# Optimization experiments

Measured on AMD Instinct MI355X. Metric: run time of the kernel, lower is better.

Reference implementation:

```python
import jax, jax.numpy as jnp
import numpy as np

B, D_IN, D_H = 8192, 2048, 2048


def _glorot(key, shape, fan_in):
    bound = 1.0 / np.sqrt(fan_in)
    return jax.random.uniform(key, shape, jnp.float32, -bound, bound)


def setup_inputs() -> dict:
    key = jax.random.key(0)
    ks = jax.random.split(key, 16)
    inp = {
        'x': jax.random.normal(ks[0], (B, D_IN), jnp.float32),
        'h': jax.random.normal(ks[1], (B, D_H), jnp.float32),
        'c': jax.random.normal(ks[2], (B, D_H), jnp.float32),
    }
    # Linear weights stored torch-style: W [out, in], y = x @ W.T + b
    names = ['Wix', 'Wmx', 'Wox']
    for i, n in enumerate(names):
        inp[n] = _glorot(ks[3 + i], (D_H, D_IN), D_IN)
        inp['b' + n[1:]] = _glorot(ks[6 + i], (D_H,), D_IN)
    names_h = ['Wih', 'Wmh', 'Woh']
    for i, n in enumerate(names_h):
        inp[n] = _glorot(ks[9 + i], (D_H, D_H), D_H)
        inp['b' + n[1:]] = _glorot(ks[12 + i], (D_H,), D_H)
    return inp


def reference(x, h, c, Wix, bix, Wmx, bmx, Wox, box, Wih, bih, Wmh, bmh, Woh, boh):
    # Fuse the 3 distinct x-GEMMs and 3 h-GEMMs into two concatenated GEMMs.
    Wx = jnp.concatenate([Wix, Wmx, Wox], axis=0)   # [3H, D_IN]
    Wh = jnp.concatenate([Wih, Wmh, Woh], axis=0)   # [3H, D_H]
    bx = jnp.concatenate([bix, bmx, box])
    bh = jnp.concatenate([bih, bmh, boh])
    g = x @ Wx.T + bx + h @ Wh.T + bh               # [B, 3H]
    gi, gm, go = jnp.split(g, 3, axis=-1)
    input_state = jax.nn.sigmoid(gi)
    # Faithful to source: memory gate pre-activation used for BOTH
    # the sigmoid "forget" gate and the tanh candidate (forgot_gate_* unused).
    forgot_state = jax.nn.sigmoid(gm)
    memory_state = jnp.tanh(gm)
    output_state = jax.nn.sigmoid(go)
    c_new = forgot_state * c + input_state * memory_state
    h_new = output_state * jnp.tanh(c_new)
    return (h_new, c_new)
```

## Files before the change

kernel.cpp:

```cpp
#include <hip/hip_runtime.h>

#define DEV __device__ __forceinline__

typedef __bf16 bf16x8 __attribute__((ext_vector_type(8)));
typedef float f32x4 __attribute__((ext_vector_type(4)));
typedef unsigned short ushort8 __attribute__((ext_vector_type(8)));

constexpr int BATCH = 8192;
constexpr int HD    = 2048;
constexpr size_t NX   = (size_t)BATCH * HD;
constexpr size_t NW   = (size_t)HD * HD;
constexpr size_t NTOT = 2 * NX + 6 * NW;

DEV unsigned short f2bf(float f) {
    unsigned int v = __builtin_bit_cast(unsigned int, f);
    unsigned int r = (v + 0x7FFFu + ((v >> 16) & 1u)) >> 16;
    return (unsigned short)r;
}
DEV float sigm(float v)  { return 1.0f / (1.0f + __expf(-v)); }
DEV float tanh_(float v) {
    float z = fminf(fmaxf(v, -15.0f), 15.0f);
    float e = __expf(2.0f * z);
    return (e - 1.0f) / (e + 1.0f);
}

DEV void gl16(const unsigned short* g, unsigned short* lds_uniform_base) {
    __builtin_amdgcn_global_load_lds(
        (const __attribute__((address_space(1))) unsigned int*)g,
        (__attribute__((address_space(3))) unsigned int*)lds_uniform_base,
        16, 0, 0);
}

struct CvtArgs { const float* src[8]; };

__global__ __launch_bounds__(256) void cvt_all(CvtArgs a, unsigned short* __restrict__ dst) {
    const size_t starts[9] = {0, NX, 2*NX, 2*NX+NW, 2*NX+2*NW, 2*NX+3*NW,
                              2*NX+4*NW, 2*NX+5*NW, NTOT};
    const size_t base = (size_t)blockIdx.x * 2048;
    int s = 0;
    while (base >= starts[s + 1]) ++s;
    const float* src = a.src[s] + (base - starts[s]) + threadIdx.x * 8;
    f32x4 u0 = *reinterpret_cast<const f32x4*>(src);
    f32x4 u1 = *reinterpret_cast<const f32x4*>(src + 4);
    ushort8 v;
#pragma unroll
    for (int j = 0; j < 4; ++j) { v[j] = f2bf(u0[j]); v[4 + j] = f2bf(u1[j]); }
    *reinterpret_cast<ushort8*>(dst + base + threadIdx.x * 8) = v;
}

__global__ __launch_bounds__(256, 2) void lstm_fast(
    const unsigned short* __restrict__ xb, const unsigned short* __restrict__ hb,
    const unsigned short* __restrict__ W0x, const unsigned short* __restrict__ W1x,
    const unsigned short* __restrict__ W2x, const unsigned short* __restrict__ W0h,
    const unsigned short* __restrict__ W1h, const unsigned short* __restrict__ W2h,
    const float* __restrict__ c,
    const float* __restrict__ bix, const float* __restrict__ bih,
    const float* __restrict__ bmx, const float* __restrict__ bmh,
    const float* __restrict__ box_, const float* __restrict__ boh,
    float* __restrict__ hout, float* __restrict__ cout)
{
    __shared__ unsigned short As [128 * 32];
    __shared__ unsigned short B0s[128 * 32];
    __shared__ unsigned short B1s[128 * 32];
    __shared__ unsigned short B2s[128 * 32];

    const int tid  = threadIdx.x;
    const int lane = tid & 63;
    const int wave = tid >> 6;

    const int n0 = blockIdx.x * 128;
    const int m0 = blockIdx.y * 128;

    const int arow = lane >> 2;
    const int acol = (lane & 3) * 8;

    const int mOff = (wave >> 1) * 64;
    const int nOff = (wave & 1) * 64;
    const int q    = lane >> 4;
    const int ml   = lane & 15;

    f32x4 a0[4][4] = {};
    f32x4 a1[4][4] = {};
    f32x4 a2[4][4] = {};

    const int r0 = wave * 32, r1 = wave * 32 + 16;

    for (int kt = 0; kt < 128; ++kt) {
        const int k0 = kt * 32;
        const unsigned short *Asrc, *W0, *W1, *W2;
        int kk;
        if (k0 < HD) { Asrc = xb; W0 = W0x; W1 = W1x; W2 = W2x; kk = k0; }
        else         { Asrc = hb; W0 = W0h; W1 = W1h; W2 = W2h; kk = k0 - HD; }

        gl16(Asrc + (size_t)(m0 + r0 + arow) * HD + kk + acol, &As [r0 * 32]);
        gl16(Asrc + (size_t)(m0 + r1 + arow) * HD + kk + acol, &As [r1 * 32]);
        gl16(W0   + (size_t)(n0 + r0 + arow) * HD + kk + acol, &B0s[r0 * 32]);
        gl16(W0   + (size_t)(n0 + r1 + arow) * HD + kk + acol, &B0s[r1 * 32]);
        gl16(W1   + (size_t)(n0 + r0 + arow) * HD + kk + acol, &B1s[r0 * 32]);
        gl16(W1   + (size_t)(n0 + r1 + arow) * HD + kk + acol, &B1s[r1 * 32]);
        gl16(W2   + (size_t)(n0 + r0 + arow) * HD + kk + acol, &B2s[r0 * 32]);
        gl16(W2   + (size_t)(n0 + r1 + arow) * HD + kk + acol, &B2s[r1 * 32]);
        __syncthreads();

        bf16x8 af[4];
#pragma unroll
        for (int t = 0; t < 4; ++t)
            af[t] = *reinterpret_cast<const bf16x8*>(&As[(mOff + t * 16 + ml) * 32 + q * 8]);

        {
            bf16x8 bfr[4];
#pragma unroll
            for (int tn = 0; tn < 4; ++tn)
                bfr[tn] = *reinterpret_cast<const bf16x8*>(&B0s[(nOff + tn * 16 + ml) * 32 + q * 8]);
#pragma unroll
            for (int tm = 0; tm < 4; ++tm)
#pragma unroll
                for (int tn = 0; tn < 4; ++tn)
                    a0[tm][tn] = __builtin_amdgcn_mfma_f32_16x16x32_bf16(af[tm], bfr[tn], a0[tm][tn], 0, 0, 0);
        }
        {
            bf16x8 bfr[4];
#pragma unroll
            for (int tn = 0; tn < 4; ++tn)
                bfr[tn] = *reinterpret_cast<const bf16x8*>(&B1s[(nOff + tn * 16 + ml) * 32 + q * 8]);
#pragma unroll
            for (int tm = 0; tm < 4; ++tm)
#pragma unroll
                for (int tn = 0; tn < 4; ++tn)
                    a1[tm][tn] = __builtin_amdgcn_mfma_f32_16x16x32_bf16(af[tm], bfr[tn], a1[tm][tn], 0, 0, 0);
        }
        {
            bf16x8 bfr[4];
#pragma unroll
            for (int tn = 0; tn < 4; ++tn)
                bfr[tn] = *reinterpret_cast<const bf16x8*>(&B2s[(nOff + tn * 16 + ml) * 32 + q * 8]);
#pragma unroll
            for (int tm = 0; tm < 4; ++tm)
#pragma unroll
                for (int tn = 0; tn < 4; ++tn)
                    a2[tm][tn] = __builtin_amdgcn_mfma_f32_16x16x32_bf16(af[tm], bfr[tn], a2[tm][tn], 0, 0, 0);
        }
        __syncthreads();
    }

#pragma unroll
    for (int tn = 0; tn < 4; ++tn) {
        const int col = n0 + nOff + tn * 16 + ml;
        const float Bi = bix[col] + bih[col];
        const float Bm = bmx[col] + bmh[col];
        const float Bo = box_[col] + boh[col];
#pragma unroll
        for (int tm = 0; tm < 4; ++tm) {
            const int rb = m0 + mOff + tm * 16 + q * 4;
#pragma unroll
            for (int r = 0; r < 4; ++r) {
                const size_t b = rb + r;
                const float cold = c[b * HD + col];
                const float gi = a0[tm][tn][r] + Bi;
                const float gm = a1[tm][tn][r] + Bm;
                const float go = a2[tm][tn][r] + Bo;
                const float i_s = sigm(gi);
                const float f_s = sigm(gm);
                const float m_s = tanh_(gm);
                const float o_s = sigm(go);
                const float cn  = f_s * cold + i_s * m_s;
                const float hn  = o_s * tanh_(cn);
                hout[b * HD + col] = hn;
                cout[b * HD + col] = cn;
            }
        }
    }
}

DEV void stage64f(unsigned short* lds, const float* src, size_t row_base, int kk, int tid) {
    const int r  = tid >> 2;
    const int cc = (tid & 3) * 8;
    const float* s = src + (row_base + r) * (size_t)HD + kk + cc;
    f32x4 u0 = *(const f32x4*)s;
    f32x4 u1 = *(const f32x4*)(s + 4);
    ushort8 v;
#pragma unroll
    for (int j = 0; j < 4; ++j) { v[j] = f2bf(u0[j]); v[4 + j] = f2bf(u1[j]); }
    *reinterpret_cast<ushort8*>(&lds[r * 32 + cc]) = v;
}

__global__ __launch_bounds__(256, 2) void lstm_slow(
    const float* __restrict__ x,   const float* __restrict__ h,
    const float* __restrict__ c,
    const float* __restrict__ Wix, const float* __restrict__ bix,
    const float* __restrict__ Wmx, const float* __restrict__ bmx,
    const float* __restrict__ Wox, const float* __restrict__ box_,
    const float* __restrict__ Wih, const float* __restrict__ bih,
    const float* __restrict__ Wmh, const float* __restrict__ bmh,
    const float* __restrict__ Woh, const float* __restrict__ boh,
    float* __restrict__ hout, float* __restrict__ cout)
{
    __shared__ unsigned short As[64 * 32];
    __shared__ unsigned short B0s[128 * 32];
    __shared__ unsigned short B1s[128 * 32];
    __shared__ unsigned short B2s[128 * 32];

    const int tid  = threadIdx.x;
    const int lane = tid & 63;
    const int wave = tid >> 6;
    const int n0 = blockIdx.x * 128;
    const int m0 = blockIdx.y * 64;
    const int mOff = (wave >> 1) * 32;
    const int nOff = (wave & 1) * 64;
    const int q    = lane >> 4;
    const int ml   = lane & 15;

    f32x4 a0[2][4] = {}; f32x4 a1[2][4] = {}; f32x4 a2[2][4] = {};

    auto kstep = [&](const float* Asrc, const float* W0, const float* W1,
                     const float* W2, int kk) {
        stage64f(As, Asrc, m0, kk, tid & 255);
        stage64f(B0s,           W0, n0,      kk, tid);
        stage64f(B0s + 64 * 32, W0, n0 + 64, kk, tid);
        stage64f(B1s,           W1, n0,      kk, tid);
        stage64f(B1s + 64 * 32, W1, n0 + 64, kk, tid);
        stage64f(B2s,           W2, n0,      kk, tid);
        stage64f(B2s + 64 * 32, W2, n0 + 64, kk, tid);
        __syncthreads();
        bf16x8 af[2], bfr[4];
        af[0] = *reinterpret_cast<const bf16x8*>(&As[(mOff      + ml) * 32 + q * 8]);
        af[1] = *reinterpret_cast<const bf16x8*>(&As[(mOff + 16 + ml) * 32 + q * 8]);
#pragma unroll
        for (int tn = 0; tn < 4; ++tn)
            bfr[tn] = *reinterpret_cast<const bf16x8*>(&B0s[(nOff + tn * 16 + ml) * 32 + q * 8]);
#pragma unroll
        for (int tm = 0; tm < 2; ++tm)
#pragma unroll
            for (int tn = 0; tn < 4; ++tn)
                a0[tm][tn] = __builtin_amdgcn_mfma_f32_16x16x32_bf16(af[tm], bfr[tn], a0[tm][tn], 0, 0, 0);
#pragma unroll
        for (int tn = 0; tn < 4; ++tn)
            bfr[tn] = *reinterpret_cast<const bf16x8*>(&B1s[(nOff + tn * 16 + ml) * 32 + q * 8]);
#pragma unroll
        for (int tm = 0; tm < 2; ++tm)
#pragma unroll
            for (int tn = 0; tn < 4; ++tn)
                a1[tm][tn] = __builtin_amdgcn_mfma_f32_16x16x32_bf16(af[tm], bfr[tn], a1[tm][tn], 0, 0, 0);
#pragma unroll
        for (int tn = 0; tn < 4; ++tn)
            bfr[tn] = *reinterpret_cast<const bf16x8*>(&B2s[(nOff + tn * 16 + ml) * 32 + q * 8]);
#pragma unroll
        for (int tm = 0; tm < 2; ++tm)
#pragma unroll
            for (int tn = 0; tn < 4; ++tn)
                a2[tm][tn] = __builtin_amdgcn_mfma_f32_16x16x32_bf16(af[tm], bfr[tn], a2[tm][tn], 0, 0, 0);
        __syncthreads();
    };

    for (int kt = 0; kt < 64; ++kt) kstep(x, Wix, Wmx, Wox, kt * 32);
    for (int kt = 0; kt < 64; ++kt) kstep(h, Wih, Wmh, Woh, kt * 32);

#pragma unroll
    for (int tn = 0; tn < 4; ++tn) {
        const int col = n0 + nOff + tn * 16 + ml;
        const float Bi = bix[col] + bih[col];
        const float Bm = bmx[col] + bmh[col];
        const float Bo = box_[col] + boh[col];
#pragma unroll
        for (int tm = 0; tm < 2; ++tm) {
            const int rb = m0 + mOff + tm * 16 + q * 4;
#pragma unroll
            for (int r = 0; r < 4; ++r) {
                const size_t b = rb + r;
                const float cold = c[b * HD + col];
                const float gi = a0[tm][tn][r] + Bi;
                const float gm = a1[tm][tn][r] + Bm;
                const float go = a2[tm][tn][r] + Bo;
                const float cn = sigm(gm) * cold + sigm(gi) * tanh_(gm);
                const float hn = sigm(go) * tanh_(cn);
                hout[b * HD + col] = hn;
                cout[b * HD + col] = cn;
            }
        }
    }
}

extern "C" void kernel_launch(void* const* d_in, const int* in_sizes, int n_in,
                              void* d_out, int out_size, void* d_ws, size_t ws_size,
                              hipStream_t stream) {
    const float* x   = (const float*)d_in[0];
    const float* h   = (const float*)d_in[1];
    const float* c   = (const float*)d_in[2];
    const float* Wix = (const float*)d_in[3];  const float* bix = (const float*)d_in[4];
    const float* Wmx = (const float*)d_in[5];  const float* bmx = (const float*)d_in[6];
    const float* Wox = (const float*)d_in[7];  const float* box_= (const float*)d_in[8];
    const float* Wih = (const float*)d_in[9];  const float* bih = (const float*)d_in[10];
    const float* Wmh = (const float*)d_in[11]; const float* bmh = (const float*)d_in[12];
    const float* Woh = (const float*)d_in[13]; const float* boh = (const float*)d_in[14];

    float* hout = (float*)d_out;
    float* cout = hout + NX;

    if (ws_size >= NTOT * sizeof(unsigned short)) {
        unsigned short* ws = (unsigned short*)d_ws;
        CvtArgs a;
        a.src[0] = x;   a.src[1] = h;
        a.src[2] = Wix; a.src[3] = Wmx; a.src[4] = Wox;
        a.src[5] = Wih; a.src[6] = Wmh; a.src[7] = Woh;
        cvt_all<<<dim3((unsigned)(NTOT / 2048)), dim3(256), 0, stream>>>(a, ws);

        const unsigned short* xb  = ws;
        const unsigned short* hb  = ws + NX;
        const unsigned short* W0x = ws + 2 * NX;
        const unsigned short* W1x = ws + 2 * NX + NW;
        const unsigned short* W2x = ws + 2 * NX + 2 * NW;
        const unsigned short* W0h = ws + 2 * NX + 3 * NW;
        const unsigned short* W1h = ws + 2 * NX + 4 * NW;
        const unsigned short* W2h = ws + 2 * NX + 5 * NW;

        lstm_fast<<<dim3(HD / 128, BATCH / 128), dim3(256), 0, stream>>>(
            xb, hb, W0x, W1x, W2x, W0h, W1h, W2h,
            c, bix, bih, bmx, bmh, box_, boh, hout, cout);
    } else {
        lstm_slow<<<dim3(HD / 128, BATCH / 64), dim3(256), 0, stream>>>(
            x, h, c, Wix, bix, Wmx, bmx, Wox, box_,
            Wih, bih, Wmh, bmh, Woh, boh, hout, cout);
    }
}
```

Before: 788.2 us.

## Double-buffer LDS tiles to overlap global loads with MFMA compute

```diff
diff --git a/kernel.cpp b/kernel.cpp
--- a/kernel.cpp
+++ b/kernel.cpp
@@ -31,17 +31,26 @@
         16, 0, 0);
 }
 
-struct CvtArgs { const float* src[8]; };
-
-__global__ __launch_bounds__(256) void cvt_all(CvtArgs a, unsigned short* __restrict__ dst) {
-    const size_t starts[9] = {0, NX, 2*NX, 2*NX+NW, 2*NX+2*NW, 2*NX+3*NW,
-                              2*NX+4*NW, 2*NX+5*NW, NTOT};
+__global__ __launch_bounds__(256) void cvt_all(
+    const float* __restrict__ x,  const float* __restrict__ h,
+    const float* __restrict__ w0, const float* __restrict__ w1,
+    const float* __restrict__ w2, const float* __restrict__ w3,
+    const float* __restrict__ w4, const float* __restrict__ w5,
+    unsigned short* __restrict__ dst)
+{
     const size_t base = (size_t)blockIdx.x * 2048;
-    int s = 0;
-    while (base >= starts[s + 1]) ++s;
-    const float* src = a.src[s] + (base - starts[s]) + threadIdx.x * 8;
-    f32x4 u0 = *reinterpret_cast<const f32x4*>(src);
-    f32x4 u1 = *reinterpret_cast<const f32x4*>(src + 4);
+    const float* src; size_t rel;
+    if      (base <  NX)          { src = x;  rel = base; }
+    else if (base < 2*NX)         { src = h;  rel = base - NX; }
+    else if (base < 2*NX +   NW)  { src = w0; rel = base - 2*NX; }
+    else if (base < 2*NX + 2*NW)  { src = w1; rel = base - (2*NX +   NW); }
+    else if (base < 2*NX + 3*NW)  { src = w2; rel = base - (2*NX + 2*NW); }
+    else if (base < 2*NX + 4*NW)  { src = w3; rel = base - (2*NX + 3*NW); }
+    else if (base < 2*NX + 5*NW)  { src = w4; rel = base - (2*NX + 4*NW); }
+    else                          { src = w5; rel = base - (2*NX + 5*NW); }
+    const float* s = src + rel + threadIdx.x * 8;
+    f32x4 u0 = *reinterpret_cast<const f32x4*>(s);
+    f32x4 u1 = *reinterpret_cast<const f32x4*>(s + 4);
     ushort8 v;
 #pragma unroll
     for (int j = 0; j < 4; ++j) { v[j] = f2bf(u0[j]); v[4 + j] = f2bf(u1[j]); }
@@ -59,10 +68,10 @@
     const float* __restrict__ box_, const float* __restrict__ boh,
     float* __restrict__ hout, float* __restrict__ cout)
 {
-    __shared__ unsigned short As [128 * 32];
-    __shared__ unsigned short B0s[128 * 32];
-    __shared__ unsigned short B1s[128 * 32];
-    __shared__ unsigned short B2s[128 * 32];
+    __shared__ unsigned short As [2][128 * 32];
+    __shared__ unsigned short B0s[2][128 * 32];
+    __shared__ unsigned short B1s[2][128 * 32];
+    __shared__ unsigned short B2s[2][128 * 32];
 
     const int tid  = threadIdx.x;
     const int lane = tid & 63;
@@ -79,39 +88,43 @@
     const int q    = lane >> 4;
     const int ml   = lane & 15;
 
+    const int r0 = wave * 32, r1 = wave * 32 + 16;
+
+    const size_t aoff0 = (size_t)(m0 + r0 + arow) * HD + acol;
+    const size_t aoff1 = (size_t)(m0 + r1 + arow) * HD + acol;
+    const size_t boff0 = (size_t)(n0 + r0 + arow) * HD + acol;
+    const size_t boff1 = (size_t)(n0 + r1 + arow) * HD + acol;
+
     f32x4 a0[4][4] = {};
     f32x4 a1[4][4] = {};
     f32x4 a2[4][4] = {};
 
-    const int r0 = wave * 32, r1 = wave * 32 + 16;
-
-    for (int kt = 0; kt < 128; ++kt) {
+    auto stage = [&](int kt, int buf) {
         const int k0 = kt * 32;
         const unsigned short *Asrc, *W0, *W1, *W2;
         int kk;
         if (k0 < HD) { Asrc = xb; W0 = W0x; W1 = W1x; W2 = W2x; kk = k0; }
         else         { Asrc = hb; W0 = W0h; W1 = W1h; W2 = W2h; kk = k0 - HD; }
-
-        gl16(Asrc + (size_t)(m0 + r0 + arow) * HD + kk + acol, &As [r0 * 32]);
-        gl16(Asrc + (size_t)(m0 + r1 + arow) * HD + kk + acol, &As [r1 * 32]);
-        gl16(W0   + (size_t)(n0 + r0 + arow) * HD + kk + acol, &B0s[r0 * 32]);
-        gl16(W0   + (size_t)(n0 + r1 + arow) * HD + kk + acol, &B0s[r1 * 32]);
-        gl16(W1   + (size_t)(n0 + r0 + arow) * HD + kk + acol, &B1s[r0 * 32]);
-        gl16(W1   + (size_t)(n0 + r1 + arow) * HD + kk + acol, &B1s[r1 * 32]);
-        gl16(W2   + (size_t)(n0 + r0 + arow) * HD + kk + acol, &B2s[r0 * 32]);
-        gl16(W2   + (size_t)(n0 + r1 + arow) * HD + kk + acol, &B2s[r1 * 32]);
-        __syncthreads();
-
+        gl16(Asrc + aoff0 + kk, &As [buf][r0 * 32]);
+        gl16(Asrc + aoff1 + kk, &As [buf][r1 * 32]);
+        gl16(W0   + boff0 + kk, &B0s[buf][r0 * 32]);
+        gl16(W0   + boff1 + kk, &B0s[buf][r1 * 32]);
+        gl16(W1   + boff0 + kk, &B1s[buf][r0 * 32]);
+        gl16(W1   + boff1 + kk, &B1s[buf][r1 * 32]);
+        gl16(W2   + boff0 + kk, &B2s[buf][r0 * 32]);
+        gl16(W2   + boff1 + kk, &B2s[buf][r1 * 32]);
+    };
+
+    auto compute = [&](int buf) {
         bf16x8 af[4];
 #pragma unroll
         for (int t = 0; t < 4; ++t)
-            af[t] = *reinterpret_cast<const bf16x8*>(&As[(mOff + t * 16 + ml) * 32 + q * 8]);
-
+            af[t] = *reinterpret_cast<const bf16x8*>(&As[buf][(mOff + t * 16 + ml) * 32 + q * 8]);
         {
             bf16x8 bfr[4];
 #pragma unroll
             for (int tn = 0; tn < 4; ++tn)
-                bfr[tn] = *reinterpret_cast<const bf16x8*>(&B0s[(nOff + tn * 16 + ml) * 32 + q * 8]);
+                bfr[tn] = *reinterpret_cast<const bf16x8*>(&B0s[buf][(nOff + tn * 16 + ml) * 32 + q * 8]);
 #pragma unroll
             for (int tm = 0; tm < 4; ++tm)
 #pragma unroll
@@ -122,7 +135,7 @@
             bf16x8 bfr[4];
 #pragma unroll
             for (int tn = 0; tn < 4; ++tn)
-                bfr[tn] = *reinterpret_cast<const bf16x8*>(&B1s[(nOff + tn * 16 + ml) * 32 + q * 8]);
+                bfr[tn] = *reinterpret_cast<const bf16x8*>(&B1s[buf][(nOff + tn * 16 + ml) * 32 + q * 8]);
 #pragma unroll
             for (int tm = 0; tm < 4; ++tm)
 #pragma unroll
@@ -133,15 +146,28 @@
             bf16x8 bfr[4];
 #pragma unroll
             for (int tn = 0; tn < 4; ++tn)
-                bfr[tn] = *reinterpret_cast<const bf16x8*>(&B2s[(nOff + tn * 16 + ml) * 32 + q * 8]);
+                bfr[tn] = *reinterpret_cast<const bf16x8*>(&B2s[buf][(nOff + tn * 16 + ml) * 32 + q * 8]);
 #pragma unroll
             for (int tm = 0; tm < 4; ++tm)
 #pragma unroll
                 for (int tn = 0; tn < 4; ++tn)
                     a2[tm][tn] = __builtin_amdgcn_mfma_f32_16x16x32_bf16(af[tm], bfr[tn], a2[tm][tn], 0, 0, 0);
         }
+    };
+
+    stage(0, 0);
+    asm volatile("s_waitcnt vmcnt(0)" ::: "memory");
+    __syncthreads();
+
+    int cur = 0;
+    for (int kt = 0; kt < 127; ++kt) {
+        stage(kt + 1, cur ^ 1);
+        compute(cur);
+        asm volatile("s_waitcnt vmcnt(0)" ::: "memory");
         __syncthreads();
+        cur ^= 1;
     }
+    compute(cur);
 
 #pragma unroll
     for (int tn = 0; tn < 4; ++tn) {
@@ -298,11 +324,8 @@
 
     if (ws_size >= NTOT * sizeof(unsigned short)) {
         unsigned short* ws = (unsigned short*)d_ws;
-        CvtArgs a;
-        a.src[0] = x;   a.src[1] = h;
-        a.src[2] = Wix; a.src[3] = Wmx; a.src[4] = Wox;
-        a.src[5] = Wih; a.src[6] = Wmh; a.src[7] = Woh;
-        cvt_all<<<dim3((unsigned)(NTOT / 2048)), dim3(256), 0, stream>>>(a, ws);
+        cvt_all<<<dim3((unsigned)(NTOT / 2048)), dim3(256), 0, stream>>>(
+            x, h, Wix, Wmx, Wox, Wih, Wmh, Woh, ws);
 
         const unsigned short* xb  = ws;
         const unsigned short* hb  = ws + NX;
```

Result: slower. 848.6 us (+7.7%).
